# Kernel optimization log

Hardware: AMD Instinct MI355X
Metric: run time of the kernel (lower is better)

Reference implementation:

```python
import jax, jax.numpy as jnp
import numpy as np
from jax import lax

B, N, AH, AW = 32, 128, 512, 512
IMG_H = IMG_W = 2048


def setup_inputs() -> dict:
    key = jax.random.key(0)
    k1, k2, k3, k4, k5, k6 = jax.random.split(key, 6)
    # sigmoid-like attention probabilities in (0,1)
    att = jax.random.uniform(k1, (B, 1, AH, AW), jnp.float32, 1e-4, 1.0 - 1e-4)
    x1 = jax.random.uniform(k2, (B, N), jnp.float32, 0.0, IMG_W * 0.7)
    y1 = jax.random.uniform(k3, (B, N), jnp.float32, 0.0, IMG_H * 0.7)
    bw = jax.random.uniform(k4, (B, N), jnp.float32, 8.0, IMG_W * 0.25)
    bh = jax.random.uniform(k5, (B, N), jnp.float32, 8.0, IMG_H * 0.25)
    x2 = jnp.minimum(x1 + bw, float(IMG_W))
    y2 = jnp.minimum(y1 + bh, float(IMG_H))
    lab = jnp.where(jax.random.uniform(k6, (B, N)) < 0.85, 0.0, -1.0)
    bboxs = jnp.stack([x1, y1, x2, y2, lab], axis=-1)
    return {"attention_mask": att, "bboxs": bboxs, "img_h": IMG_H, "img_w": IMG_W}


def reference(attention_mask, bboxs, img_h, img_w):
    Bn, _, Ah, Aw = attention_mask.shape
    f32 = attention_mask.dtype
    sx = Aw / img_w
    sy = Ah / img_h
    labels = bboxs[:, :, 4]
    c = bboxs[:, :, :4]
    # validity: label != -1 and all coords within image (torch filters sequentially == AND)
    valid = (labels != -1.0) & (c[:, :, 0] <= img_w) & (c[:, :, 1] <= img_h) \
            & (c[:, :, 2] <= img_w) & (c[:, :, 3] <= img_h)
    scaled = c * jnp.array([sx, sy, sx, sy], dtype=f32)  # [B,N,4] in attention coords
    xs = jnp.arange(Aw)
    ys = jnp.arange(Ah)

    def per_image(att, boxes, vmask):
        def step(mask, bv):
            box, v = bv
            bx1, by1, bx2, by2 = box[0], box[1], box[2], box[3]
            fx1 = jnp.floor(bx1); fy1 = jnp.floor(by1)
            x1m = fx1 + 1.0 - bx1; y1m = fy1 + 1.0 - by1          # anti-alias edge margins
            x2m = bx2 - jnp.floor(bx2); y2m = by2 - jnp.floor(by2)
            x1 = jnp.maximum(fx1, 0.0).astype(jnp.int32)
            y1 = jnp.maximum(fy1, 0.0).astype(jnp.int32)
            x2 = jnp.minimum(jnp.ceil(bx2) + 1.0, Aw).astype(jnp.int32)
            y2 = jnp.minimum(jnp.ceil(by2) + 1.0, Ah).astype(jnp.int32)
            one = jnp.ones((), f32)
            colw = jnp.where(xs == x1, x1m, one) * jnp.where(xs == x2 - 1, x2m, one)
            roww = jnp.where(ys == y1, y1m, one) * jnp.where(ys == y2 - 1, y2m, one)
            inb = (((ys >= y1) & (ys < y2))[:, None]) & (((xs >= x1) & (xs < x2))[None, :])
            val = roww[:, None] * colw[None, :]
            # later boxes overwrite earlier ones inside their region (matches torch slice-assign)
            mask = jnp.where(v & inb, val, mask)
            return mask, None

        mask_gt, _ = lax.scan(step, jnp.zeros((Ah, Aw), f32), (boxes, vmask))
        p = att[0]
        # BCE with torch-style log clamping at -100
        log_p = jnp.maximum(jnp.log(p), -100.0)
        log_1mp = jnp.maximum(jnp.log1p(-p), -100.0)
        bce = -jnp.mean(mask_gt * log_p + (1.0 - mask_gt) * log_1mp)
        return jnp.where(jnp.any(vmask), bce, jnp.zeros((), f32))

    losses = jax.vmap(per_image)(attention_mask, scaled, valid)
    return jnp.mean(losses, axis=0, keepdims=True)
```

## Files before the change

### kernel.cpp

```cpp
#include <hip/hip_runtime.h>
#include <hip/hip_bf16.h>

#define B_   32
#define N_   128
#define AH_  512
#define AW_  512
#define LCAP 64

#define CFENCE() asm volatile("" ::: "memory")

__global__ __launch_bounds__(128) void row_bce_kernel(
    const float* __restrict__ att,
    const float* __restrict__ bboxs,
    const int*   __restrict__ img_h_p,
    const int*   __restrict__ img_w_p,
    float*       __restrict__ wave_sums)
{
    const int t    = threadIdx.x;
    const int lane = t & 63;
    const int wid  = t >> 6;
    const int task = (blockIdx.x << 1) | wid;
    const int b    = task >> 8;
    const int y0   = (task & 255) << 1;

    __shared__ float4 s_geo[2][LCAP];
    __shared__ float2 s_rv [2][LCAP];
    __shared__ float  s_mask[2][2][AW_];

    const float fw  = (float)(*img_w_p);
    const float fh  = (float)(*img_h_p);
    const float sxs = (float)AW_ / fw;
    const float sys = (float)AH_ / fh;

    const float4* p4 = (const float4*)(att + ((size_t)b * AH_ + y0) * AW_);
    float4 P[2][2];
    #pragma unroll
    for (int r = 0; r < 2; ++r)
        #pragma unroll
        for (int h = 0; h < 2; ++h)
            P[r][h] = p4[r * 128 + h * 64 + lane];

    bool  act_any[2];
    int   actb[2];
    int   gx1[2], gx2[2];
    float gx1m[2], gx2m[2];
    float rv0[2], rv1[2];
    #pragma unroll
    for (int k = 0; k < 2; ++k) {
        const int n = lane + 64 * k;
        const float* bp = bboxs + ((size_t)b * N_ + n) * 5;
        const float c0 = bp[0], c1 = bp[1], c2 = bp[2], c3 = bp[3], lab = bp[4];
        const bool valid = (lab != -1.0f) && (c0 <= fw) && (c1 <= fh)
                                          && (c2 <= fw) && (c3 <= fh);
        const float bx1 = c0 * sxs, by1 = c1 * sys;
        const float bx2 = c2 * sxs, by2 = c3 * sys;
        const float fx1 = floorf(bx1), fy1 = floorf(by1);
        const float x1m = fx1 + 1.0f - bx1;
        const float y1m = fy1 + 1.0f - by1;
        const float x2m = bx2 - floorf(bx2);
        const float y2m = by2 - floorf(by2);
        const int x1 = (int)fmaxf(fx1, 0.0f);
        const int y1 = (int)fmaxf(fy1, 0.0f);
        const int x2 = (int)fminf(ceilf(bx2) + 1.0f, (float)AW_);
        const int y2 = (int)fminf(ceilf(by2) + 1.0f, (float)AH_);
        gx1[k] = x1; gx2[k] = x2; gx1m[k] = x1m; gx2m[k] = x2m;
        int ab = 0;
        #pragma unroll
        for (int r = 0; r < 2; ++r) {
            const int y = y0 + r;
            const bool a = valid && (y >= y1) && (y < y2);
            ab |= a ? (1 << r) : 0;
            const float rw = ((y == y1)     ? y1m : 1.0f)
                           * ((y == y2 - 1) ? y2m : 1.0f);
            if (r == 0) rv0[k] = rw; else rv1[k] = rw;
        }
        actb[k]    = ab;
        act_any[k] = (ab != 0);
    }

    const unsigned long long ltm = (1ull << lane) - 1ull;
    const unsigned long long bal[2] = { __ballot(act_any[0]), __ballot(act_any[1]) };
    const bool have = (bal[0] | bal[1]) != 0ull;

    float*  m0    = s_mask[wid][0];
    float*  m1    = s_mask[wid][1];
    float4* mrow4 = (float4*)s_mask[wid];

    if (have) {
        const float4 z = make_float4(0.f, 0.f, 0.f, 0.f);
        #pragma unroll
        for (int q = 0; q < 4; ++q) mrow4[lane + 64 * q] = z;
        CFENCE();

        #pragma unroll
        for (int k = 0; k < 2; ++k) {
            const int cnt = __popcll(bal[k]);
            if (cnt == 0) continue;
            if (act_any[k]) {
                const int slot = __popcll(bal[k] & ltm);
                s_geo[wid][slot] = make_float4(
                    __int_as_float(gx1[k] | (gx2[k] << 16)),
                    gx1m[k], gx2m[k], __int_as_float(actb[k]));
                s_rv[wid][slot] = make_float2(rv0[k], rv1[k]);
            }
            CFENCE();

            float4 g_cur = s_geo[wid][0];
            float2 v_cur = s_rv[wid][0];
            for (int i = 0; i < cnt; ++i) {
                const float4 g = g_cur;
                const float2 v = v_cur;
                if (i + 1 < cnt) {
                    g_cur = s_geo[wid][i + 1];
                    v_cur = s_rv[wid][i + 1];
                }
                const int px = __float_as_int(g.x);
                const int e1 = px & 0xffff;
                const int e2 = px >> 16;
                const int ab = __float_as_int(g.w);
                for (int x = e1 + lane; x < e2; x += 64) {
                    const float edge = ((x == e1)     ? g.y : 1.0f)
                                     * ((x == e2 - 1) ? g.z : 1.0f);
                    if (ab & 1) m0[x] = v.x * edge;
                    if (ab & 2) m1[x] = v.y * edge;
                }
            }
            CFENCE();
        }
    }

    float acc = 0.0f;
    #pragma unroll
    for (int r = 0; r < 2; ++r) {
        #pragma unroll
        for (int h = 0; h < 2; ++h) {
            const float4 p = P[r][h];
            float4 m = make_float4(0.f, 0.f, 0.f, 0.f);
            if (have) m = mrow4[r * 128 + h * 64 + lane];
            const float pv[4] = {p.x, p.y, p.z, p.w};
            const float mv[4] = {m.x, m.y, m.z, m.w};
            const bool nz = (m.x != 0.f) | (m.y != 0.f)
                          | (m.z != 0.f) | (m.w != 0.f);
            if (__any(nz)) {
                #pragma unroll
                for (int j = 0; j < 4; ++j) {
                    const float lp = __logf(pv[j]);
                    const float l1 = __logf(1.0f - pv[j]);
                    acc += l1 + mv[j] * (lp - l1);
                }
            } else {
                #pragma unroll
                for (int j = 0; j < 4; ++j)
                    acc += __logf(1.0f - pv[j]);
            }
        }
    }

    #pragma unroll
    for (int off = 32; off; off >>= 1) acc += __shfl_down(acc, off, 64);
    if (lane == 0) wave_sums[task] = acc;
}

__global__ __launch_bounds__(1024) void final_kernel(
    const float* __restrict__ bboxs,
    const int*   __restrict__ img_h_p,
    const int*   __restrict__ img_w_p,
    const float* __restrict__ wave_sums,
    float*       __restrict__ out)
{
    const int t = threadIdx.x;
    const int b = t >> 5;
    const int j = t & 31;

    __shared__ float s_sum[1024];
    __shared__ int   s_any[1024];
    __shared__ float s_loss[B_];

    float s = 0.0f;
    #pragma unroll
    for (int k = 0; k < 8; ++k) s += wave_sums[b * 256 + j + 32 * k];
    s_sum[t] = s;

    const float fw = (float)(*img_w_p);
    const float fh = (float)(*img_h_p);
    int av = 0;
    const float* bp = bboxs + (size_t)b * N_ * 5;
    #pragma unroll
    for (int n = j * 4; n < j * 4 + 4; ++n) {
        const float c0 = bp[n * 5 + 0];
        const float c1 = bp[n * 5 + 1];
        const float c2 = bp[n * 5 + 2];
        const float c3 = bp[n * 5 + 3];
        const float lab = bp[n * 5 + 4];
        av |= ((lab != -1.0f) && (c0 <= fw) && (c1 <= fh)
                              && (c2 <= fw) && (c3 <= fh)) ? 1 : 0;
    }
    s_any[t] = av;
    __syncthreads();

    if (j == 0) {
        float sum = 0.0f;
        int anyv = 0;
        for (int k = 0; k < 32; ++k) {
            sum  += s_sum[b * 32 + k];
            anyv |= s_any[b * 32 + k];
        }
        s_loss[b] = anyv ? (-sum * (1.0f / (float)(AH_ * AW_))) : 0.0f;
    }
    __syncthreads();

    if (t == 0) {
        float total = 0.0f;
        for (int k = 0; k < B_; ++k) total += s_loss[k];
        out[0] = total * (1.0f / (float)B_);
    }
}

extern "C" void kernel_launch(void* const* d_in, const int* in_sizes, int n_in,
                              void* d_out, int out_size, void* d_ws, size_t ws_size,
                              hipStream_t stream)
{
    const float* att   = (const float*)d_in[0];
    const float* bboxs = (const float*)d_in[1];
    const int*   img_h = (const int*)d_in[2];
    const int*   img_w = (const int*)d_in[3];
    float* out = (float*)d_out;
    float* wave_sums = (float*)d_ws;

    row_bce_kernel<<<B_ * AH_ / 4, 128, 0, stream>>>(att, bboxs, img_h, img_w, wave_sums);
    final_kernel<<<1, 1024, 0, stream>>>(bboxs, img_h, img_w, wave_sums, out);
}
```

Baseline: 29.36 us.

## Keep per-row mask in registers instead of shared memory rasterization

Replaces the shared-memory mask rows with a per-lane register array holding 8 columns per row at stride 64. Each box is applied with wave-uniform column-chunk bounds obtained through readfirstlane. This removes the LDS zero-fill, the scattered stores and the read-back. Attention loads become scalar strided float loads issued after mask construction instead of float4 prefetched loads. Both box halves are merged into one compacted list with packed geometry and an occupancy hint of 8 blocks. The cost is more predicated ALU work per box and a later, narrower load of the probabilities.

Result: slower. 41.01 us (+39.7%).

```diff
diff --git a/kernel.cpp b/kernel.cpp
--- a/kernel.cpp
+++ b/kernel.cpp
@@ -5,11 +5,11 @@
 #define N_   128
 #define AH_  512
 #define AW_  512
-#define LCAP 64
+#define LCAP 128
 
 #define CFENCE() asm volatile("" ::: "memory")
 
-__global__ __launch_bounds__(128) void row_bce_kernel(
+__global__ __launch_bounds__(128, 8) void row_bce_kernel(
     const float* __restrict__ att,
     const float* __restrict__ bboxs,
     const int*   __restrict__ img_h_p,
@@ -23,28 +23,17 @@
     const int b    = task >> 8;
     const int y0   = (task & 255) << 1;
 
-    __shared__ float4 s_geo[2][LCAP];
-    __shared__ float2 s_rv [2][LCAP];
-    __shared__ float  s_mask[2][2][AW_];
+    __shared__ unsigned s_pk[2][LCAP];
+    __shared__ float4   s_wt[2][LCAP];
 
     const float fw  = (float)(*img_w_p);
     const float fh  = (float)(*img_h_p);
     const float sxs = (float)AW_ / fw;
     const float sys = (float)AH_ / fh;
 
-    const float4* p4 = (const float4*)(att + ((size_t)b * AH_ + y0) * AW_);
-    float4 P[2][2];
-    #pragma unroll
-    for (int r = 0; r < 2; ++r)
-        #pragma unroll
-        for (int h = 0; h < 2; ++h)
-            P[r][h] = p4[r * 128 + h * 64 + lane];
-
-    bool  act_any[2];
-    int   actb[2];
-    int   gx1[2], gx2[2];
-    float gx1m[2], gx2m[2];
-    float rv0[2], rv1[2];
+    bool     act_any[2];
+    unsigned pk[2];
+    float4   wt[2];
     #pragma unroll
     for (int k = 0; k < 2; ++k) {
         const int n = lane + 64 * k;
@@ -63,8 +52,8 @@
         const int y1 = (int)fmaxf(fy1, 0.0f);
         const int x2 = (int)fminf(ceilf(bx2) + 1.0f, (float)AW_);
         const int y2 = (int)fminf(ceilf(by2) + 1.0f, (float)AH_);
-        gx1[k] = x1; gx2[k] = x2; gx1m[k] = x1m; gx2m[k] = x2m;
-        int ab = 0;
+        int   ab = 0;
+        float rv0 = 1.0f, rv1 = 1.0f;
         #pragma unroll
         for (int r = 0; r < 2; ++r) {
             const int y = y0 + r;
@@ -72,86 +61,79 @@
             ab |= a ? (1 << r) : 0;
             const float rw = ((y == y1)     ? y1m : 1.0f)
                            * ((y == y2 - 1) ? y2m : 1.0f);
-            if (r == 0) rv0[k] = rw; else rv1[k] = rw;
-        }
-        actb[k]    = ab;
+            if (r == 0) rv0 = rw; else rv1 = rw;
+        }
         act_any[k] = (ab != 0);
+        pk[k] = (unsigned)x1 | ((unsigned)x2 << 10) | ((unsigned)ab << 20);
+        wt[k] = make_float4(x1m, x2m, rv0, rv1);
     }
 
     const unsigned long long ltm = (1ull << lane) - 1ull;
-    const unsigned long long bal[2] = { __ballot(act_any[0]), __ballot(act_any[1]) };
-    const bool have = (bal[0] | bal[1]) != 0ull;
-
-    float*  m0    = s_mask[wid][0];
-    float*  m1    = s_mask[wid][1];
-    float4* mrow4 = (float4*)s_mask[wid];
-
-    if (have) {
-        const float4 z = make_float4(0.f, 0.f, 0.f, 0.f);
+    const unsigned long long bal0 = __ballot(act_any[0]);
+    const unsigned long long bal1 = __ballot(act_any[1]);
+    const int cnt0 = __popcll(bal0);
+    const int cnt  = cnt0 + __popcll(bal1);
+    if (act_any[0]) {
+        const int s = __popcll(bal0 & ltm);
+        s_pk[wid][s] = pk[0];
+        s_wt[wid][s] = wt[0];
+    }
+    if (act_any[1]) {
+        const int s = cnt0 + __popcll(bal1 & ltm);
+        s_pk[wid][s] = pk[1];
+        s_wt[wid][s] = wt[1];
+    }
+    CFENCE();
+
+    float val[2][8];
+    #pragma unroll
+    for (int r = 0; r < 2; ++r)
         #pragma unroll
-        for (int q = 0; q < 4; ++q) mrow4[lane + 64 * q] = z;
-        CFENCE();
-
-        #pragma unroll
-        for (int k = 0; k < 2; ++k) {
-            const int cnt = __popcll(bal[k]);
-            if (cnt == 0) continue;
-            if (act_any[k]) {
-                const int slot = __popcll(bal[k] & ltm);
-                s_geo[wid][slot] = make_float4(
-                    __int_as_float(gx1[k] | (gx2[k] << 16)),
-                    gx1m[k], gx2m[k], __int_as_float(actb[k]));
-                s_rv[wid][slot] = make_float2(rv0[k], rv1[k]);
+        for (int h = 0; h < 8; ++h) val[r][h] = 0.0f;
+
+    if (cnt > 0) {
+        unsigned pkc = s_pk[wid][0];
+        float4   wtc = s_wt[wid][0];
+        for (int i = 0; i < cnt; ++i) {
+            const unsigned pki = pkc;
+            const float4   wti = wtc;
+            if (i + 1 < cnt) {
+                pkc = s_pk[wid][i + 1];
+                wtc = s_wt[wid][i + 1];
             }
-            CFENCE();
-
-            float4 g_cur = s_geo[wid][0];
-            float2 v_cur = s_rv[wid][0];
-            for (int i = 0; i < cnt; ++i) {
-                const float4 g = g_cur;
-                const float2 v = v_cur;
-                if (i + 1 < cnt) {
-                    g_cur = s_geo[wid][i + 1];
-                    v_cur = s_rv[wid][i + 1];
-                }
-                const int px = __float_as_int(g.x);
-                const int e1 = px & 0xffff;
-                const int e2 = px >> 16;
-                const int ab = __float_as_int(g.w);
-                for (int x = e1 + lane; x < e2; x += 64) {
-                    const float edge = ((x == e1)     ? g.y : 1.0f)
-                                     * ((x == e2 - 1) ? g.z : 1.0f);
-                    if (ab & 1) m0[x] = v.x * edge;
-                    if (ab & 2) m1[x] = v.y * edge;
+            const unsigned pks = __builtin_amdgcn_readfirstlane(pki);
+            const int e1 = (int)(pks & 1023u);
+            const int e2 = (int)((pks >> 10) & 1023u);
+            const int ab = (int)(pks >> 20);
+            const int h1 = e1 >> 6;
+            const int h2 = (e2 - 1) >> 6;
+            #pragma unroll
+            for (int h = 0; h < 8; ++h) {
+                if (h >= h1 && h <= h2) {
+                    const int  x   = (h << 6) + lane;
+                    const bool inb = (x >= e1) & (x < e2);
+                    const float edge = ((x == e1)     ? wti.x : 1.0f)
+                                     * ((x == e2 - 1) ? wti.y : 1.0f);
+                    if (ab & 1) val[0][h] = inb ? wti.z * edge : val[0][h];
+                    if (ab & 2) val[1][h] = inb ? wti.w * edge : val[1][h];
                 }
             }
-            CFENCE();
-        }
-    }
-
+        }
+    }
+
+    const float* prow = att + ((size_t)b * AH_ + y0) * AW_;
     float acc = 0.0f;
     #pragma unroll
     for (int r = 0; r < 2; ++r) {
         #pragma unroll
-        for (int h = 0; h < 2; ++h) {
-            const float4 p = P[r][h];
-            float4 m = make_float4(0.f, 0.f, 0.f, 0.f);
-            if (have) m = mrow4[r * 128 + h * 64 + lane];
-            const float pv[4] = {p.x, p.y, p.z, p.w};
-            const float mv[4] = {m.x, m.y, m.z, m.w};
-            const bool nz = (m.x != 0.f) | (m.y != 0.f)
-                          | (m.z != 0.f) | (m.w != 0.f);
-            if (__any(nz)) {
-                #pragma unroll
-                for (int j = 0; j < 4; ++j) {
-                    const float lp = __logf(pv[j]);
-                    const float l1 = __logf(1.0f - pv[j]);
-                    acc += l1 + mv[j] * (lp - l1);
-                }
+        for (int h = 0; h < 8; ++h) {
+            const float p  = prow[r * AW_ + (h << 6) + lane];
+            const float mv = val[r][h];
+            const float l1 = __logf(1.0f - p);
+            if (__any(mv != 0.0f)) {
+                acc += l1 + mv * (__logf(p) - l1);
             } else {
-                #pragma unroll
-                for (int j = 0; j < 4; ++j)
-                    acc += __logf(1.0f - pv[j]);
+                acc += l1;
             }
         }
     }
```

## Fuse final reduction into main kernel via last-block atomic counter

Applied to the files above, without the earlier changes.

Removes the separate final reduction kernel. Each block writes its partial sum, bumps a global atomic counter, and the last block to finish does the per-image and batch reduction. Also switches to log2 with a single ln2 rescale, packs box bounds and the active-row bits into one word read with readfirstlane, and issues the attention loads before the scalar setup. The launch cost of the second kernel is traded for a memset node, atomics, and a serial tail in one block.

After: 96.13 us. 227% more time.

```diff
diff --git a/kernel.cpp b/kernel.cpp
--- a/kernel.cpp
+++ b/kernel.cpp
@@ -6,6 +6,7 @@
 #define AH_  512
 #define AW_  512
 #define LCAP 64
+#define LN2  0.6931471805599453f
 
 #define CFENCE() asm volatile("" ::: "memory")
 
@@ -14,7 +15,9 @@
     const float* __restrict__ bboxs,
     const int*   __restrict__ img_h_p,
     const int*   __restrict__ img_w_p,
-    float*       __restrict__ wave_sums)
+    float*       __restrict__ block_sums,
+    unsigned*    __restrict__ counter,
+    float*       __restrict__ out)
 {
     const int t    = threadIdx.x;
     const int lane = t & 63;
@@ -26,19 +29,21 @@
     __shared__ float4 s_geo[2][LCAP];
     __shared__ float2 s_rv [2][LCAP];
     __shared__ float  s_mask[2][2][AW_];
+    __shared__ float  s_bsum[2];
+    __shared__ int    s_last;
+
+    const float4* p4 = (const float4*)(att + ((size_t)b * AH_ + y0) * AW_);
+    float4 P[2][2];
+    #pragma unroll
+    for (int r = 0; r < 2; ++r)
+        #pragma unroll
+        for (int h = 0; h < 2; ++h)
+            P[r][h] = p4[r * 128 + h * 64 + lane];
 
     const float fw  = (float)(*img_w_p);
     const float fh  = (float)(*img_h_p);
     const float sxs = (float)AW_ / fw;
     const float sys = (float)AH_ / fh;
-
-    const float4* p4 = (const float4*)(att + ((size_t)b * AH_ + y0) * AW_);
-    float4 P[2][2];
-    #pragma unroll
-    for (int r = 0; r < 2; ++r)
-        #pragma unroll
-        for (int h = 0; h < 2; ++h)
-            P[r][h] = p4[r * 128 + h * 64 + lane];
 
     bool  act_any[2];
     int   actb[2];
@@ -78,13 +83,14 @@
         act_any[k] = (ab != 0);
     }
 
-    const unsigned long long ltm = (1ull << lane) - 1ull;
-    const unsigned long long bal[2] = { __ballot(act_any[0]), __ballot(act_any[1]) };
-    const bool have = (bal[0] | bal[1]) != 0ull;
-
-    float*  m0    = s_mask[wid][0];
-    float*  m1    = s_mask[wid][1];
-    float4* mrow4 = (float4*)s_mask[wid];
+    const unsigned long long ltm  = (1ull << lane) - 1ull;
+    const unsigned long long bal0 = __ballot(act_any[0]);
+    const unsigned long long bal1 = __ballot(act_any[1]);
+    const bool have = (bal0 | bal1) != 0ull;
+
+    float* m0 = s_mask[wid][0];
+    float* m1 = s_mask[wid][1];
+    float4* mrow4 = (float4*)m0;
 
     if (have) {
         const float4 z = make_float4(0.f, 0.f, 0.f, 0.f);
@@ -94,30 +100,31 @@
 
         #pragma unroll
         for (int k = 0; k < 2; ++k) {
-            const int cnt = __popcll(bal[k]);
+            const unsigned long long bal = (k == 0) ? bal0 : bal1;
+            const int cnt = __popcll(bal);
             if (cnt == 0) continue;
             if (act_any[k]) {
-                const int slot = __popcll(bal[k] & ltm);
+                const int slot = __popcll(bal & ltm);
                 s_geo[wid][slot] = make_float4(
-                    __int_as_float(gx1[k] | (gx2[k] << 16)),
-                    gx1m[k], gx2m[k], __int_as_float(actb[k]));
+                    __int_as_float(gx1[k] | (gx2[k] << 10) | (actb[k] << 20)),
+                    gx1m[k], gx2m[k], 0.0f);
                 s_rv[wid][slot] = make_float2(rv0[k], rv1[k]);
             }
             CFENCE();
 
             float4 g_cur = s_geo[wid][0];
             float2 v_cur = s_rv[wid][0];
-            for (int i = 0; i < cnt; ++i) {
+            for (int j = 0; j < cnt; ++j) {
                 const float4 g = g_cur;
                 const float2 v = v_cur;
-                if (i + 1 < cnt) {
-                    g_cur = s_geo[wid][i + 1];
-                    v_cur = s_rv[wid][i + 1];
+                if (j + 1 < cnt) {
+                    g_cur = s_geo[wid][j + 1];
+                    v_cur = s_rv[wid][j + 1];
                 }
-                const int px = __float_as_int(g.x);
-                const int e1 = px & 0xffff;
-                const int e2 = px >> 16;
-                const int ab = __float_as_int(g.w);
+                const int px = __builtin_amdgcn_readfirstlane(__float_as_int(g.x));
+                const int e1 = px & 1023;
+                const int e2 = (px >> 10) & 1023;
+                const int ab = px >> 20;
                 for (int x = e1 + lane; x < e2; x += 64) {
                     const float edge = ((x == e1)     ? g.y : 1.0f)
                                      * ((x == e2 - 1) ? g.z : 1.0f);
@@ -144,75 +151,69 @@
             if (__any(nz)) {
                 #pragma unroll
                 for (int j = 0; j < 4; ++j) {
-                    const float lp = __logf(pv[j]);
-                    const float l1 = __logf(1.0f - pv[j]);
+                    const float lp = __log2f(pv[j]);
+                    const float l1 = __log2f(1.0f - pv[j]);
                     acc += l1 + mv[j] * (lp - l1);
                 }
             } else {
                 #pragma unroll
                 for (int j = 0; j < 4; ++j)
-                    acc += __logf(1.0f - pv[j]);
+                    acc += __log2f(1.0f - pv[j]);
             }
         }
     }
 
     #pragma unroll
     for (int off = 32; off; off >>= 1) acc += __shfl_down(acc, off, 64);
-    if (lane == 0) wave_sums[task] = acc;
-}
-
-__global__ __launch_bounds__(1024) void final_kernel(
-    const float* __restrict__ bboxs,
-    const int*   __restrict__ img_h_p,
-    const int*   __restrict__ img_w_p,
-    const float* __restrict__ wave_sums,
-    float*       __restrict__ out)
-{
-    const int t = threadIdx.x;
-    const int b = t >> 5;
-    const int j = t & 31;
-
-    __shared__ float s_sum[1024];
-    __shared__ int   s_any[1024];
-    __shared__ float s_loss[B_];
-
-    float s = 0.0f;
-    #pragma unroll
-    for (int k = 0; k < 8; ++k) s += wave_sums[b * 256 + j + 32 * k];
-    s_sum[t] = s;
-
-    const float fw = (float)(*img_w_p);
-    const float fh = (float)(*img_h_p);
-    int av = 0;
-    const float* bp = bboxs + (size_t)b * N_ * 5;
-    #pragma unroll
-    for (int n = j * 4; n < j * 4 + 4; ++n) {
-        const float c0 = bp[n * 5 + 0];
-        const float c1 = bp[n * 5 + 1];
-        const float c2 = bp[n * 5 + 2];
-        const float c3 = bp[n * 5 + 3];
-        const float lab = bp[n * 5 + 4];
-        av |= ((lab != -1.0f) && (c0 <= fw) && (c1 <= fh)
-                              && (c2 <= fw) && (c3 <= fh)) ? 1 : 0;
-    }
-    s_any[t] = av;
+    if (lane == 0) s_bsum[wid] = acc;
     __syncthreads();
-
-    if (j == 0) {
-        float sum = 0.0f;
-        int anyv = 0;
-        for (int k = 0; k < 32; ++k) {
-            sum  += s_sum[b * 32 + k];
-            anyv |= s_any[b * 32 + k];
-        }
-        s_loss[b] = anyv ? (-sum * (1.0f / (float)(AH_ * AW_))) : 0.0f;
+    if (t == 0) {
+        block_sums[blockIdx.x] = s_bsum[0] + s_bsum[1];
+        __threadfence();
+        const unsigned old = atomicAdd(counter, 1u);
+        s_last = (old == (unsigned)(gridDim.x - 1)) ? 1 : 0;
     }
     __syncthreads();
 
-    if (t == 0) {
-        float total = 0.0f;
-        for (int k = 0; k < B_; ++k) total += s_loss[k];
-        out[0] = total * (1.0f / (float)B_);
+    if (s_last) {
+        __threadfence();
+        const int bb = t >> 2;
+        const int j  = t & 3;
+        float s = 0.0f;
+        #pragma unroll
+        for (int k = 0; k < 32; ++k)
+            s += block_sums[bb * 128 + j * 32 + k];
+
+        int av = 0;
+        const float* bp = bboxs + ((size_t)bb * N_ + j * 32) * 5;
+        for (int n = 0; n < 32; ++n) {
+            const float c0 = bp[n * 5 + 0];
+            const float c1 = bp[n * 5 + 1];
+            const float c2 = bp[n * 5 + 2];
+            const float c3 = bp[n * 5 + 3];
+            const float lb = bp[n * 5 + 4];
+            av |= ((lb != -1.0f) && (c0 <= fw) && (c1 <= fh)
+                                 && (c2 <= fw) && (c3 <= fh)) ? 1 : 0;
+        }
+
+        __shared__ float s_s[128];
+        __shared__ int   s_a[128];
+        __shared__ float s_loss[B_];
+        s_s[t] = s;
+        s_a[t] = av;
+        __syncthreads();
+        if (t < B_) {
+            const float sum = s_s[4*t] + s_s[4*t+1] + s_s[4*t+2] + s_s[4*t+3];
+            const int  anyv = s_a[4*t] | s_a[4*t+1] | s_a[4*t+2] | s_a[4*t+3];
+            s_loss[t] = anyv ? (-sum * (LN2 / (float)(AH_ * AW_))) : 0.0f;
+        }
+        __syncthreads();
+        if (t == 0) {
+            float total = 0.0f;
+            #pragma unroll
+            for (int k = 0; k < B_; ++k) total += s_loss[k];
+            out[0] = total * (1.0f / (float)B_);
+        }
     }
 }
 
@@ -225,8 +226,11 @@
     const int*   img_h = (const int*)d_in[2];
     const int*   img_w = (const int*)d_in[3];
     float* out = (float*)d_out;
-    float* wave_sums = (float*)d_ws;
-
-    row_bce_kernel<<<B_ * AH_ / 4, 128, 0, stream>>>(att, bboxs, img_h, img_w, wave_sums);
-    final_kernel<<<1, 1024, 0, stream>>>(bboxs, img_h, img_w, wave_sums, out);
+
+    float*    block_sums = (float*)d_ws;
+    unsigned* counter    = (unsigned*)(block_sums + 4096);
+
+    hipMemsetAsync(counter, 0, sizeof(unsigned), stream);
+    row_bce_kernel<<<B_ * AH_ / 4, 128, 0, stream>>>(
+        att, bboxs, img_h, img_w, block_sums, counter, out);
 }
```
